# Kernel optimization log

Measured on AMD Instinct MI355X. Metric: run time of the kernel, lower is better.

The kernel has to match this reference:

```python
import jax, jax.numpy as jnp
from jax import lax
import numpy as np
from functools import reduce

# --- module hyperparameters (init_kwargs defaults) ---
T_LOW = 0.5; T_HIGH = 0.9; SIGMAS = (1.0, 2.0); BETA = 0.5
Z_RADIUS = 1; XY_RADIUS = 0; DUST_MIN_SIZE = 100; EPS = 1e-7
MAX_HYST_ITERS = 256   # flood-fill iteration cap (converges far earlier on real data)
MAX_CC_ITERS = 256     # label-propagation iteration cap


def _gauss_kernel(sigma):
    # separable gaussian, truncate at 3 sigma (standard scipy convention)
    r = int(3.0 * sigma + 0.5)
    x = np.arange(-r, r + 1, dtype=np.float32)
    k = np.exp(-(x * x) / (2.0 * sigma * sigma))
    return jnp.asarray(k / k.sum())


def _conv1d_axis(v, k, axis):
    # 'same' zero-padded 1D correlation along `axis` of a 3D volume
    r = k.shape[0] // 2
    pad = [(0, 0)] * 3; pad[axis] = (r, r)
    vp = jnp.pad(v, pad)
    n = v.shape[axis]
    out = jnp.zeros_like(v)
    for i in range(k.shape[0]):  # tiny fixed tap loop, vectorized over the volume
        sl = [slice(None)] * 3; sl[axis] = slice(i, i + n)
        out = out + k[i] * vp[tuple(sl)]
    return out


def _shifts6(x, pad_val):
    # 6-connected neighbor views (cross connectivity, matches ndi default)
    p = jnp.pad(x, 1, constant_values=pad_val)
    c = slice(1, -1)
    return (p[:-2, c, c], p[2:, c, c], p[c, :-2, c], p[c, 2:, c], p[c, c, :-2], p[c, c, 2:])


def _axis_morph(m, axis, radius, dilate):
    # box dilation/erosion along one axis (box SE is separable)
    op = jnp.logical_or if dilate else jnp.logical_and
    pad_val = (not dilate)
    for _ in range(radius):
        pad = [(1, 1) if a == axis else (0, 0) for a in range(3)]
        p = jnp.pad(m, pad, constant_values=pad_val)
        lo = tuple(slice(0, -2) if a == axis else slice(None) for a in range(3))
        hi = tuple(slice(2, None) if a == axis else slice(None) for a in range(3))
        m = op(op(m, p[lo]), p[hi])
    return m


def _hysteresis(vol):
    # keep low-threshold voxels connected to a high-threshold voxel (flood fill)
    low = vol > T_LOW
    high = vol > T_HIGH
    def body(st):
        m, _, i = st
        nm = m
        for s in _shifts6(m, False):
            nm = nm | s
        nm = nm & low
        return nm, jnp.any(nm != m), i + 1
    mask, _, _ = lax.while_loop(lambda st: st[1] & (st[2] < MAX_HYST_ITERS), body,
                                (high, jnp.bool_(True), jnp.int32(0)))
    return mask


def _closing(mask):
    # anisotropic binary closing with box SE (2*z_r+1, 2*xy_r+1, 2*xy_r+1)
    for axis, r in ((0, Z_RADIUS), (1, XY_RADIUS), (2, XY_RADIUS)):
        mask = _axis_morph(mask, axis, r, dilate=True)
    for axis, r in ((0, Z_RADIUS), (1, XY_RADIUS), (2, XY_RADIUS)):
        mask = _axis_morph(mask, axis, r, dilate=False)
    return mask


def _remove_small(mask):
    # connected-component labeling via max-label propagation, then size filter
    n = mask.size
    idx = jnp.arange(1, n + 1, dtype=jnp.int32).reshape(mask.shape)
    lab0 = jnp.where(mask, idx, 0)
    def body(st):
        l, _, i = st
        nl = l
        for s in _shifts6(l, 0):
            nl = jnp.maximum(nl, s)
        nl = jnp.where(mask, nl, 0)
        return nl, jnp.any(nl != l), i + 1
    lab, _, _ = lax.while_loop(lambda st: st[1] & (st[2] < MAX_CC_ITERS), body,
                               (lab0, jnp.bool_(True), jnp.int32(0)))
    counts = jax.ops.segment_sum(mask.ravel().astype(jnp.int32), lab.ravel(), num_segments=n + 1)
    return mask & (counts[lab] >= DUST_MIN_SIZE)


def _process_volume(v):
    d2 = jnp.asarray([1.0, -2.0, 1.0], v.dtype)
    surfs = []
    for sigma in SIGMAS:
        k = _gauss_kernel(sigma)
        s = v
        for ax in range(3):
            s = _conv1d_axis(s, k, ax)
        scale = sigma * sigma
        fxx = _conv1d_axis(s, d2, 0) * scale
        fyy = _conv1d_axis(s, d2, 1) * scale
        fzz = _conv1d_axis(s, d2, 2) * scale
        surf = jnp.exp(-(fxx * fxx + fyy * fyy) / (BETA * BETA * (fzz * fzz + EPS))) * jnp.abs(fzz)
        mx = surf.max()
        surfs.append(jnp.where(mx > 0, surf / (mx + EPS), jnp.zeros_like(surf)))
    surfaceness = reduce(jnp.maximum, surfs)  # max over sigma stack
    vol = lax.stop_gradient(v * surfaceness)  # binarization pipeline is piecewise constant
    mask = _hysteresis(vol)
    mask = _closing(mask)
    if DUST_MIN_SIZE > 0:
        mask = _remove_small(mask)
    return mask.astype(v.dtype)


def setup_inputs() -> dict:
    key = jax.random.key(0)
    outputs = jax.random.uniform(key, (2, 192, 192, 192), dtype=jnp.float32)
    return {"outputs": outputs}


def reference(outputs):
    return jax.vmap(_process_volume)(outputs)
```

## Files before the change

### kernel.cpp

```cpp
#include <hip/hip_runtime.h>
#include <cmath>

#define D3   192
#define SZP  (D3*D3)
#define NVOX (D3*D3*D3)
#define NTOT (2*NVOX)
#define NBLK (NTOT/256)
#define W3   (NTOT/64)
#define WBLK (W3/256)
#define NSUM (W3/64)
#define NQ   (NTOT/4)
#define NQB  (NQ/256)
#define BPB  (NVOX/256)

#define HT 16
#define HH 8
#define HL (HT+2*HH)
#define HLDS (HL*HL*3)
#define NHT  (12*12*2)

typedef unsigned long long u64;

struct Taps13 { float k[13]; };

__device__ __forceinline__ void coords(int idx, int& x, int& y, int& z, int& b) {
  x = idx % D3;
  y = (idx / D3) % D3;
  z = (idx / SZP) % D3;
  b = idx / NVOX;
}

template<int AXIS, int R>
__global__ void __launch_bounds__(256) conv1d_k(const float* __restrict__ in,
                                                float* __restrict__ out, Taps13 t) {
  int idx = blockIdx.x * 256 + threadIdx.x;
  int x, y, z, b; coords(idx, x, y, z, b);
  int c = (AXIS == 0) ? z : (AXIS == 1) ? y : x;
  const int stride = (AXIS == 0) ? SZP : (AXIS == 1) ? D3 : 1;
  float acc = 0.f;
#pragma unroll
  for (int i = -R; i <= R; ++i) {
    int cc = c + i;
    if (cc >= 0 && cc < D3)
      acc = __fadd_rn(acc, __fmul_rn(t.k[i + R], in[idx + i * stride]));
  }
  out[idx] = acc;
}

__global__ void __launch_bounds__(256) surf_k(const float* __restrict__ s,
                                              float* __restrict__ surf,
                                              float* __restrict__ bmax,
                                              float scale) {
  int idx = blockIdx.x * 256 + threadIdx.x;
  int x, y, z, b; coords(idx, x, y, z, b);
  float ctr = s[idx];
  float fxx, fyy, fzz;
  { float acc = 0.f;
    if (z > 0)      acc = __fadd_rn(acc, __fmul_rn(1.f, s[idx - SZP]));
    acc = __fadd_rn(acc, __fmul_rn(-2.f, ctr));
    if (z < D3 - 1) acc = __fadd_rn(acc, __fmul_rn(1.f, s[idx + SZP]));
    fxx = __fmul_rn(acc, scale); }
  { float acc = 0.f;
    if (y > 0)      acc = __fadd_rn(acc, __fmul_rn(1.f, s[idx - D3]));
    acc = __fadd_rn(acc, __fmul_rn(-2.f, ctr));
    if (y < D3 - 1) acc = __fadd_rn(acc, __fmul_rn(1.f, s[idx + D3]));
    fyy = __fmul_rn(acc, scale); }
  { float acc = 0.f;
    if (x > 0)      acc = __fadd_rn(acc, __fmul_rn(1.f, s[idx - 1]));
    acc = __fadd_rn(acc, __fmul_rn(-2.f, ctr));
    if (x < D3 - 1) acc = __fadd_rn(acc, __fmul_rn(1.f, s[idx + 1]));
    fzz = __fmul_rn(acc, scale); }

  float num = __fadd_rn(__fmul_rn(fxx, fxx), __fmul_rn(fyy, fyy));
  float den = __fmul_rn(0.25f, __fadd_rn(__fmul_rn(fzz, fzz), 1e-7f));
  float arg = __fdiv_rn(-num, den);
  float sv  = __fmul_rn(expf(arg), fabsf(fzz));
  surf[idx] = sv;

  float m = sv;
  #pragma unroll
  for (int off = 32; off > 0; off >>= 1) m = fmaxf(m, __shfl_down(m, off));
  __shared__ float wred[4];
  int lane = threadIdx.x & 63, wid = threadIdx.x >> 6;
  if (lane == 0) wred[wid] = m;
  __syncthreads();
  if (threadIdx.x == 0)
    bmax[blockIdx.x] = fmaxf(fmaxf(wred[0], wred[1]), fmaxf(wred[2], wred[3]));
}

__global__ void __launch_bounds__(256) reduce_max_k(const float* __restrict__ bmax,
                                                    unsigned int* __restrict__ mxp) {
  int b = blockIdx.x;
  const float* p = bmax + b * BPB;
  float m = 0.f;
  for (int i = threadIdx.x; i < BPB; i += 256) m = fmaxf(m, p[i]);
  #pragma unroll
  for (int off = 32; off > 0; off >>= 1) m = fmaxf(m, __shfl_down(m, off));
  __shared__ float wred[4];
  int lane = threadIdx.x & 63, wid = threadIdx.x >> 6;
  if (lane == 0) wred[wid] = m;
  __syncthreads();
  if (threadIdx.x == 0)
    mxp[b] = __float_as_uint(fmaxf(fmaxf(wred[0], wred[1]), fmaxf(wred[2], wred[3])));
}

__global__ void __launch_bounds__(256) mask_init_pack_k(const float* __restrict__ v,
                                                        const float* __restrict__ s1,
                                                        const float* __restrict__ s2,
                                                        const unsigned int* __restrict__ mx,
                                                        u64* __restrict__ lowW,
                                                        u64* __restrict__ mW) {
  int idx = blockIdx.x * 256 + threadIdx.x;
  int b = idx / NVOX;
  float m1 = __uint_as_float(mx[b]);
  float m2 = __uint_as_float(mx[2 + b]);
  float n1 = (m1 > 0.f) ? __fdiv_rn(s1[idx], __fadd_rn(m1, 1e-7f)) : 0.f;
  float n2 = (m2 > 0.f) ? __fdiv_rn(s2[idx], __fadd_rn(m2, 1e-7f)) : 0.f;
  float vol = __fmul_rn(v[idx], fmaxf(n1, n2));
  u64 bl = __ballot(vol > 0.5f);
  u64 bh = __ballot(vol > 0.9f);
  if ((threadIdx.x & 63) == 0) {
    lowW[idx >> 6] = bl;
    mW[idx >> 6]   = bh;
  }
}

__global__ void __launch_bounds__(256) hyst8_k(const u64* __restrict__ src,
                                               u64* __restrict__ dst,
                                               const u64* __restrict__ lowW,
                                               const int* __restrict__ fprev,
                                               int* __restrict__ fcur,
                                               int* __restrict__ chg, int iter) {
  if (iter > 0 && chg[iter - 1] == 0) return;
  const int r = blockIdx.x + 12 * blockIdx.y + 144 * blockIdx.z;
  if (iter > 0) {
    bool act = false;
    for (int dz = -1; dz <= 1 && !act; ++dz) {
      int zz = (int)blockIdx.y + dz; if (zz < 0 || zz >= 12) continue;
      for (int dy = -1; dy <= 1; ++dy) {
        int yy = (int)blockIdx.x + dy; if (yy < 0 || yy >= 12) continue;
        if (fprev[yy + 12 * zz + 144 * blockIdx.z]) { act = true; break; }
      }
    }
    if (!act) { if (threadIdx.x == 0) fcur[r] = 0; return; }
  }

  __shared__ u64 sA[HLDS], sB[HLDS];
  __shared__ int blkC;
  const int t = threadIdx.x;
  if (t == 0) blkC = 0;
  const int y0 = blockIdx.x * HT - HH;
  const int z0 = blockIdx.y * HT - HH;
  const int b  = blockIdx.z;

  u64 lowr[4][3], orig[4][3];
#pragma unroll
  for (int j = 0; j < 4; ++j) {
    int l = t + 256 * j;
    int yy = l & 31, zz = l >> 5;
    int y = y0 + yy, z = z0 + zz;
    bool in = (y >= 0 && y < D3 && z >= 0 && z < D3);
    int wb = 3 * y + 576 * z + 110592 * b;
#pragma unroll
    for (int xw = 0; xw < 3; ++xw) {
      u64 sv = in ? src[wb + xw]  : 0ull;
      u64 lv = in ? lowW[wb + xw] : 0ull;
      sA[l * 3 + xw] = sv;
      orig[j][xw] = sv;
      lowr[j][xw] = lv;
    }
  }
  __syncthreads();

  u64* cur = sA; u64* nxt = sB;
  for (int s = 0; s < 8; ++s) {
#pragma unroll
    for (int j = 0; j < 4; ++j) {
      int l = t + 256 * j;
      int yy = l & 31, zz = l >> 5;
      int base = l * 3;
      u64 w0 = cur[base], w1 = cur[base + 1], w2 = cur[base + 2];
      u64 n0 = w0 | (w0 << 1) | (w0 >> 1) | (w1 << 63);
      u64 n1 = w1 | (w1 << 1) | (w1 >> 1) | (w0 >> 63) | (w2 << 63);
      u64 n2 = w2 | (w2 << 1) | (w2 >> 1) | (w1 >> 63);
      if (yy > 0)  { n0 |= cur[base - 3];  n1 |= cur[base - 2];  n2 |= cur[base - 1]; }
      if (yy < 31) { n0 |= cur[base + 3];  n1 |= cur[base + 4];  n2 |= cur[base + 5]; }
      if (zz > 0)  { n0 |= cur[base - 96]; n1 |= cur[base - 95]; n2 |= cur[base - 94]; }
      if (zz < 31) { n0 |= cur[base + 96]; n1 |= cur[base + 97]; n2 |= cur[base + 98]; }
      nxt[base]     = n0 & lowr[j][0];
      nxt[base + 1] = n1 & lowr[j][1];
      nxt[base + 2] = n2 & lowr[j][2];
    }
    __syncthreads();
    u64* tmp = cur; cur = nxt; nxt = tmp;
  }

  bool ch = false;
#pragma unroll
  for (int j = 0; j < 4; ++j) {
    int l = t + 256 * j;
    int yy = l & 31, zz = l >> 5;
    if (yy >= HH && yy < HH + HT && zz >= HH && zz < HH + HT) {
      int y = y0 + yy, z = z0 + zz;
      int wb = 3 * y + 576 * z + 110592 * b;
#pragma unroll
      for (int xw = 0; xw < 3; ++xw) {
        u64 o = cur[l * 3 + xw];
        ch |= (o != orig[j][xw]);
        dst[wb + xw] = o;
      }
    }
  }
  if (ch) blkC = 1;
  __syncthreads();
  if (t == 0) { fcur[r] = blkC; if (blkC) chg[iter] = 1; }
}

__global__ void __launch_bounds__(256) close_z_k(const u64* __restrict__ mi,
                                                 u64* __restrict__ mo) {
  int w = blockIdx.x * 256 + threadIdx.x;
  int z = (w / 576) % D3;
  u64 c   = mi[w];
  u64 zm1 = (z > 0)      ? mi[w - 576]  : 0ull;
  u64 zm2 = (z > 1)      ? mi[w - 1152] : 0ull;
  u64 zp1 = (z < D3 - 1) ? mi[w + 576]  : 0ull;
  u64 zp2 = (z < D3 - 2) ? mi[w + 1152] : 0ull;
  u64 d0 = c | zm1 | zp1;
  u64 e  = d0;
  if (z > 0)      e &= (zm2 | zm1 | c);
  if (z < D3 - 1) e &= (c | zp1 | zp2);
  mo[w] = e;
}

__global__ void __launch_bounds__(256) label_init_k(const u64* __restrict__ closedW,
                                                    int* __restrict__ lab) {
  int idx = blockIdx.x * 256 + threadIdx.x;
  int bit = (int)((closedW[idx >> 6] >> (idx & 63)) & 1ull);
  lab[idx] = bit ? (idx % NVOX) + 1 : 0;
}

__device__ __forceinline__ int imax2(int a, int b) { return a > b ? a : b; }

__global__ void __launch_bounds__(256) cc_word_k(const int* __restrict__ src,
                                                 int* __restrict__ dst,
                                                 const u64* __restrict__ chgPrev,
                                                 u64* __restrict__ chgCur,
                                                 const u64* __restrict__ sumPrev,
                                                 u64* __restrict__ sumCur,
                                                 const u64* __restrict__ closedW,
                                                 int* __restrict__ chg, int iter) {
  if (iter > 0 && chg[iter - 1] == 0) return;
  __shared__ int blkC;
  if (threadIdx.x == 0) blkC = 0;
  __syncthreads();

  const int w = blockIdx.x * 256 + threadIdx.x;
  const int xw = w % 3;
  const int y  = (w / 3) % D3;
  const int z  = (w / 576) % D3;

  u64 F, U;
  if (iter == 0) {
    F = ~0ull; U = 0ull;
  } else {
    u64 c  = ((sumPrev[w >> 6] >> (w & 63)) & 1ull) ? chgPrev[w] : 0ull;
    u64 cl = 0ull, cr = 0ull, ym = 0ull, yp = 0ull, zm = 0ull, zp = 0ull;
    if (xw > 0      && ((sumPrev[(w - 1) >> 6]   >> ((w - 1) & 63))   & 1ull)) cl = chgPrev[w - 1];
    if (xw < 2      && ((sumPrev[(w + 1) >> 6]   >> ((w + 1) & 63))   & 1ull)) cr = chgPrev[w + 1];
    if (y > 0       && ((sumPrev[(w - 3) >> 6]   >> ((w - 3) & 63))   & 1ull)) ym = chgPrev[w - 3];
    if (y < D3 - 1  && ((sumPrev[(w + 3) >> 6]   >> ((w + 3) & 63))   & 1ull)) yp = chgPrev[w + 3];
    if (z > 0       && ((sumPrev[(w - 576) >> 6] >> ((w - 576) & 63)) & 1ull)) zm = chgPrev[w - 576];
    if (z < D3 - 1  && ((sumPrev[(w + 576) >> 6] >> ((w + 576) & 63)) & 1ull)) zp = chgPrev[w + 576];
    u64 nb = (c << 1) | (c >> 1) | (cl >> 63) | (cr << 63) | ym | yp | zm | zp;
    if ((nb | c) == 0ull) { F = 0ull; U = 0ull; }
    else {
      u64 cw = closedW[w];
      F = nb & cw;
      U = c & cw & ~F;
    }
  }

  u64 P = F | U;
  u64 newc = 0;
  if (P) {
    int idx0 = xw * 64 + D3 * y + SZP * z + (w / 110592) * NVOX;
#pragma unroll
    for (int q = 0; q < 16; ++q) {
      if (!((P >> (4 * q)) & 0xFull)) continue;
      int idx = idx0 + 4 * q;
      int4 s = *(const int4*)(src + idx);
      int4 o = s;
      if ((F >> (4 * q)) & 0xFull) {
        int x = xw * 64 + 4 * q;
        const int4 z4 = make_int4(0, 0, 0, 0);
        int4 yv = (y > 0)      ? *(const int4*)(src + idx - D3)  : z4;
        int4 yw = (y < D3 - 1) ? *(const int4*)(src + idx + D3)  : z4;
        int4 zv = (z > 0)      ? *(const int4*)(src + idx - SZP) : z4;
        int4 zw = (z < D3 - 1) ? *(const int4*)(src + idx + SZP) : z4;
        int lf = (x > 0)       ? src[idx - 1] : 0;
        int rt = (x < D3 - 4)  ? src[idx + 4] : 0;
        o.x = s.x ? imax2(imax2(imax2(s.x, lf),  imax2(s.y, yv.x)), imax2(imax2(yw.x, zv.x), zw.x)) : 0;
        o.y = s.y ? imax2(imax2(imax2(s.y, s.x), imax2(s.z, yv.y)), imax2(imax2(yw.y, zv.y), zw.y)) : 0;
        o.z = s.z ? imax2(imax2(imax2(s.z, s.y), imax2(s.w, yv.z)), imax2(imax2(yw.z, zv.z), zw.z)) : 0;
        o.w = s.w ? imax2(imax2(imax2(s.w, s.z), imax2(rt,  yv.w)), imax2(imax2(yw.w, zv.w), zw.w)) : 0;
      }
      *(int4*)(dst + idx) = o;
      u64 df = (u64)((o.x != s.x) | ((o.y != s.y) << 1) |
                     ((o.z != s.z) << 2) | ((o.w != s.w) << 3));
      newc |= df << (4 * q);
    }
  }

  u64 bal = __ballot(newc != 0ull);
  if (newc) chgCur[w] = newc;
  if ((threadIdx.x & 63) == 0) sumCur[w >> 6] = bal;
  if (bal) blkC = 1;
  __syncthreads();
  if (threadIdx.x == 0 && blkC) chg[iter] = 1;
}

__global__ void __launch_bounds__(256) count_k(const int* __restrict__ lab,
                                               unsigned int* __restrict__ counts) {
  int q = blockIdx.x * 256 + threadIdx.x;
  int idx = q << 2;
  int b = idx / NVOX;
  int4 L = *(const int4*)(lab + idx);
  unsigned int* cb = counts + b * NVOX;
  if (L.x > 0) atomicAdd(&cb[L.x - 1], 1u);
  if (L.y > 0) atomicAdd(&cb[L.y - 1], 1u);
  if (L.z > 0) atomicAdd(&cb[L.z - 1], 1u);
  if (L.w > 0) atomicAdd(&cb[L.w - 1], 1u);
}

__global__ void __launch_bounds__(256) final_k(const int* __restrict__ lab,
                                               const unsigned int* __restrict__ counts,
                                               float* __restrict__ out) {
  int q = blockIdx.x * 256 + threadIdx.x;
  int idx = q << 2;
  int b = idx / NVOX;
  int4 L = *(const int4*)(lab + idx);
  const unsigned int* cb = counts + b * NVOX;
  float4 rr;
  rr.x = (L.x > 0 && cb[L.x - 1] >= 100u) ? 1.f : 0.f;
  rr.y = (L.y > 0 && cb[L.y - 1] >= 100u) ? 1.f : 0.f;
  rr.z = (L.z > 0 && cb[L.z - 1] >= 100u) ? 1.f : 0.f;
  rr.w = (L.w > 0 && cb[L.w - 1] >= 100u) ? 1.f : 0.f;
  *(float4*)(out + idx) = rr;
}

static float np_sum_f32(const float* a, int n) {
  if (n < 8) { float res = 0.f; for (int i = 0; i < n; i++) res += a[i]; return res; }
  float r[8]; for (int j = 0; j < 8; j++) r[j] = a[j];
  int i = 8;
  for (; i < n - (n % 8); i += 8) for (int j = 0; j < 8; j++) r[j] += a[i + j];
  float res = ((r[0] + r[1]) + (r[2] + r[3])) + ((r[4] + r[5]) + (r[6] + r[7]));
  for (; i < n; i++) res += a[i];
  return res;
}

extern "C" void kernel_launch(void* const* d_in, const int* in_sizes, int n_in,
                              void* d_out, int out_size, void* d_ws, size_t ws_size,
                              hipStream_t stream) {
  const float* v = (const float*)d_in[0];
  float* out = (float*)d_out;
  char* base = (char*)d_ws;
  const size_t SZBUF = (size_t)NTOT * 4;
  const size_t SZW   = (size_t)W3 * 8;

  float* A  = (float*)base;
  float* Cf = (float*)(base + SZBUF);
  unsigned int* mx = (unsigned int*)(base + 2 * SZBUF);
  float* bmax = (float*)(base + 2 * SZBUF + 256);
  float* Bf = (float*)d_out;

  u64* lowW    = (u64*)base;
  u64* mWA     = (u64*)(base + SZW);
  u64* mWB     = (u64*)(base + 2 * SZW);
  u64* closedW = (u64*)(base + 3 * SZW);
  u64* chgWA   = (u64*)(base + 4 * SZW);
  u64* chgWB   = (u64*)(base + 5 * SZW);
  u64* sumA    = (u64*)(base + 6 * SZW);
  u64* sumB    = sumA + NSUM;
  int* chgH = (int*)(sumB + NSUM);
  int* chgC = chgH + 32;
  int* hF0  = chgC + 256;
  int* hF1  = hF0 + NHT;

  int* labA = (int*)Bf;
  int* labB = (int*)Cf;
  unsigned int* counts = (unsigned int*)Cf;

  dim3 g(NBLK), gw(WBLK), gq(NQB), blk(256);

  const double sigmas[2] = {1.0, 2.0};
  for (int si = 0; si < 2; ++si) {
    double sigma = sigmas[si];
    int r = (int)(3.0 * sigma + 0.5);
    int n = 2 * r + 1;
    float a[13], k[13];
    for (int i = 0; i < n; i++) {
      float xx = (float)(i - r);
      float t  = xx * xx;
      float arg = -(t) / (float)(2.0 * sigma * sigma);
      a[i] = (float)std::exp((double)arg);
    }
    float ssum = np_sum_f32(a, n);
    for (int i = 0; i < n; i++) k[i] = a[i] / ssum;

    Taps13 T = {};
    for (int i = 0; i < n; i++) T.k[i] = k[i];
    float scale = (float)(sigma * sigma);
    float* starget = (si == 0) ? Cf : Bf;

    if (r == 3) {
      conv1d_k<0, 3><<<g, blk, 0, stream>>>(v,  A,  T);
      conv1d_k<1, 3><<<g, blk, 0, stream>>>(A,  Bf, T);
      conv1d_k<2, 3><<<g, blk, 0, stream>>>(Bf, A,  T);
    } else {
      conv1d_k<0, 6><<<g, blk, 0, stream>>>(v,  A,  T);
      conv1d_k<1, 6><<<g, blk, 0, stream>>>(A,  Bf, T);
      conv1d_k<2, 6><<<g, blk, 0, stream>>>(Bf, A,  T);
    }
    surf_k<<<g, blk, 0, stream>>>(A, starget, bmax, scale);
    reduce_max_k<<<dim3(2), blk, 0, stream>>>(bmax, mx + 2 * si);
  }

  hipMemsetAsync(chgH, 0, (32 + 256) * 4, stream);
  mask_init_pack_k<<<g, blk, 0, stream>>>(v, Cf, Bf, mx, lowW, mWA);

  for (int it = 0; it < 32; ++it) {
    const u64* s = (it & 1) ? mWB : mWA;
    u64*       d = (it & 1) ? mWA : mWB;
    const int* fp = (it & 1) ? hF0 : hF1;
    int*       fc = (it & 1) ? hF1 : hF0;
    hyst8_k<<<dim3(12, 12, 2), blk, 0, stream>>>(s, d, lowW, fp, fc, chgH, it);
  }

  close_z_k<<<gw, blk, 0, stream>>>(mWA, closedW);

  label_init_k<<<g, blk, 0, stream>>>(closedW, labA);
  for (int it = 0; it < 256; ++it) {
    const int* s = (it & 1) ? labB : labA;
    int*       d = (it & 1) ? labA : labB;
    const u64* cp = (it & 1) ? chgWB : chgWA;
    u64*       cc = (it & 1) ? chgWA : chgWB;
    const u64* sp = (it & 1) ? sumB : sumA;
    u64*       sc = (it & 1) ? sumA : sumB;
    cc_word_k<<<gw, blk, 0, stream>>>(s, d, cp, cc, sp, sc, closedW, chgC, it);
  }

  hipMemsetAsync(counts, 0, SZBUF, stream);
  count_k<<<gq, blk, 0, stream>>>(labA, counts);
  final_k<<<gq, blk, 0, stream>>>(labA, counts, out);
}
```

Before: 1.867 ms.

## Fuse hysteresis, closing, labeling and dust removal into one persistent cooperative kernel

Replaces the roughly 290 per-iteration kernel launches for hysteresis, z-closing, label init, connected-component propagation, counting and final masking with a single cooperative persistent kernel of 256 blocks. Phases are separated by a hand-written flag-based grid barrier, and the loops exit early once an iteration reports no change. The closing is fused into label init, so the closedW buffer and its mask in the CC step are dropped. This removes launch and early-return overhead but limits parallelism to 256 blocks, which loop over tiles and words, and adds global-barrier latency per iteration.

```diff
diff --git a/kernel.cpp b/kernel.cpp
--- a/kernel.cpp
+++ b/kernel.cpp
@@ -7,7 +7,7 @@
 #define NTOT (2*NVOX)
 #define NBLK (NTOT/256)
 #define W3   (NTOT/64)
-#define WBLK (W3/256)
+#define WGRP (W3/256)
 #define NSUM (W3/64)
 #define NQ   (NTOT/4)
 #define NQB  (NQ/256)
@@ -18,6 +18,9 @@
 #define HL (HT+2*HH)
 #define HLDS (HL*HL*3)
 #define NHT  (12*12*2)
+
+#define GBLK 256
+#define TT   (GBLK*256)
 
 typedef unsigned long long u64;
 
@@ -125,227 +128,274 @@
   }
 }
 
-__global__ void __launch_bounds__(256) hyst8_k(const u64* __restrict__ src,
-                                               u64* __restrict__ dst,
-                                               const u64* __restrict__ lowW,
-                                               const int* __restrict__ fprev,
-                                               int* __restrict__ fcur,
-                                               int* __restrict__ chg, int iter) {
-  if (iter > 0 && chg[iter - 1] == 0) return;
-  const int r = blockIdx.x + 12 * blockIdx.y + 144 * blockIdx.z;
-  if (iter > 0) {
-    bool act = false;
-    for (int dz = -1; dz <= 1 && !act; ++dz) {
-      int zz = (int)blockIdx.y + dz; if (zz < 0 || zz >= 12) continue;
-      for (int dy = -1; dy <= 1; ++dy) {
-        int yy = (int)blockIdx.x + dy; if (yy < 0 || yy >= 12) continue;
-        if (fprev[yy + 12 * zz + 144 * blockIdx.z]) { act = true; break; }
-      }
+struct Flag { int v; int pad[15]; };
+
+struct PipeArgs {
+  const u64* lowW; u64* mWA; u64* mWB;
+  int* labA; int* labB;
+  u64* chgWA; u64* chgWB; u64* sumA; u64* sumB;
+  int* chgH; int* chgC; int* hF0; int* hF1;
+  Flag* arr; int* go;
+  float* outp;
+};
+
+__device__ __forceinline__ int imax2(int a, int b) { return a > b ? a : b; }
+
+__device__ __forceinline__ void gbar(Flag* arr, int* go, int rnd) {
+  __syncthreads();
+  if (threadIdx.x == 0) {
+    __threadfence();
+    __hip_atomic_store(&arr[blockIdx.x].v, rnd, __ATOMIC_RELEASE, __HIP_MEMORY_SCOPE_AGENT);
+  }
+  if (blockIdx.x == 0) {
+    while (__hip_atomic_load(&arr[threadIdx.x].v, __ATOMIC_ACQUIRE,
+                             __HIP_MEMORY_SCOPE_AGENT) < rnd)
+      __builtin_amdgcn_s_sleep(1);
+    __syncthreads();
+    if (threadIdx.x == 0) {
+      __threadfence();
+      __hip_atomic_store(go, rnd, __ATOMIC_RELEASE, __HIP_MEMORY_SCOPE_AGENT);
     }
-    if (!act) { if (threadIdx.x == 0) fcur[r] = 0; return; }
-  }
-
+  } else if (threadIdx.x == 0) {
+    while (__hip_atomic_load(go, __ATOMIC_ACQUIRE, __HIP_MEMORY_SCOPE_AGENT) < rnd)
+      __builtin_amdgcn_s_sleep(1);
+  }
+  __syncthreads();
+}
+
+__global__ void __launch_bounds__(256, 1) pipeline_k(PipeArgs a) {
   __shared__ u64 sA[HLDS], sB[HLDS];
   __shared__ int blkC;
   const int t = threadIdx.x;
-  if (t == 0) blkC = 0;
-  const int y0 = blockIdx.x * HT - HH;
-  const int z0 = blockIdx.y * HT - HH;
-  const int b  = blockIdx.z;
-
-  u64 lowr[4][3], orig[4][3];
-#pragma unroll
-  for (int j = 0; j < 4; ++j) {
-    int l = t + 256 * j;
-    int yy = l & 31, zz = l >> 5;
-    int y = y0 + yy, z = z0 + zz;
-    bool in = (y >= 0 && y < D3 && z >= 0 && z < D3);
-    int wb = 3 * y + 576 * z + 110592 * b;
-#pragma unroll
-    for (int xw = 0; xw < 3; ++xw) {
-      u64 sv = in ? src[wb + xw]  : 0ull;
-      u64 lv = in ? lowW[wb + xw] : 0ull;
-      sA[l * 3 + xw] = sv;
-      orig[j][xw] = sv;
-      lowr[j][xw] = lv;
+  const int gtid = blockIdx.x * 256 + t;
+  int rnd = 0;
+
+  u64* hsrc = a.mWA; u64* hdst = a.mWB;
+  int* fp = a.hF1;   int* fc = a.hF0;
+  for (int it = 0; it < 32; ++it) {
+    for (int vt = blockIdx.x; vt < NHT; vt += GBLK) {
+      int tyi = vt % 12, tzi = (vt / 12) % 12, tb = vt / 144;
+      bool act = true;
+      if (it > 0) {
+        act = false;
+        for (int dz = -1; dz <= 1 && !act; ++dz) {
+          int zz = tzi + dz; if (zz < 0 || zz >= 12) continue;
+          for (int dy = -1; dy <= 1; ++dy) {
+            int yy = tyi + dy; if (yy < 0 || yy >= 12) continue;
+            if (fp[yy + 12 * zz + 144 * tb]) { act = true; break; }
+          }
+        }
+      }
+      if (!act) { if (t == 0) fc[vt] = 0; continue; }
+
+      if (t == 0) blkC = 0;
+      __syncthreads();
+      const int y0 = tyi * HT - HH;
+      const int z0 = tzi * HT - HH;
+
+      u64 lowr[4][3], orig[4][3];
+#pragma unroll
+      for (int j = 0; j < 4; ++j) {
+        int l = t + 256 * j;
+        int yy = l & 31, zz = l >> 5;
+        int y = y0 + yy, z = z0 + zz;
+        bool in = (y >= 0 && y < D3 && z >= 0 && z < D3);
+        int wb = 3 * y + 576 * z + 110592 * tb;
+#pragma unroll
+        for (int xw = 0; xw < 3; ++xw) {
+          u64 sv = in ? hsrc[wb + xw]   : 0ull;
+          u64 lv = in ? a.lowW[wb + xw] : 0ull;
+          sA[l * 3 + xw] = sv;
+          orig[j][xw] = sv;
+          lowr[j][xw] = lv;
+        }
+      }
+      __syncthreads();
+
+      u64* cur = sA; u64* nxt = sB;
+      for (int s = 0; s < 8; ++s) {
+#pragma unroll
+        for (int j = 0; j < 4; ++j) {
+          int l = t + 256 * j;
+          int yy = l & 31, zz = l >> 5;
+          int base = l * 3;
+          u64 w0 = cur[base], w1 = cur[base + 1], w2 = cur[base + 2];
+          u64 n0 = w0 | (w0 << 1) | (w0 >> 1) | (w1 << 63);
+          u64 n1 = w1 | (w1 << 1) | (w1 >> 1) | (w0 >> 63) | (w2 << 63);
+          u64 n2 = w2 | (w2 << 1) | (w2 >> 1) | (w1 >> 63);
+          if (yy > 0)  { n0 |= cur[base - 3];  n1 |= cur[base - 2];  n2 |= cur[base - 1]; }
+          if (yy < 31) { n0 |= cur[base + 3];  n1 |= cur[base + 4];  n2 |= cur[base + 5]; }
+          if (zz > 0)  { n0 |= cur[base - 96]; n1 |= cur[base - 95]; n2 |= cur[base - 94]; }
+          if (zz < 31) { n0 |= cur[base + 96]; n1 |= cur[base + 97]; n2 |= cur[base + 98]; }
+          nxt[base]     = n0 & lowr[j][0];
+          nxt[base + 1] = n1 & lowr[j][1];
+          nxt[base + 2] = n2 & lowr[j][2];
+        }
+        __syncthreads();
+        u64* tmp = cur; cur = nxt; nxt = tmp;
+      }
+
+      bool ch = false;
+#pragma unroll
+      for (int j = 0; j < 4; ++j) {
+        int l = t + 256 * j;
+        int yy = l & 31, zz = l >> 5;
+        if (yy >= HH && yy < HH + HT && zz >= HH && zz < HH + HT) {
+          int y = y0 + yy, z = z0 + zz;
+          int wb = 3 * y + 576 * z + 110592 * tb;
+#pragma unroll
+          for (int xw = 0; xw < 3; ++xw) {
+            u64 o = cur[l * 3 + xw];
+            ch |= (o != orig[j][xw]);
+            hdst[wb + xw] = o;
+          }
+        }
+      }
+      if (ch) blkC = 1;
+      __syncthreads();
+      if (t == 0) {
+        fc[vt] = blkC;
+        if (blkC) __hip_atomic_store(&a.chgH[it], 1, __ATOMIC_RELAXED, __HIP_MEMORY_SCOPE_AGENT);
+      }
     }
-  }
-  __syncthreads();
-
-  u64* cur = sA; u64* nxt = sB;
-  for (int s = 0; s < 8; ++s) {
-#pragma unroll
-    for (int j = 0; j < 4; ++j) {
-      int l = t + 256 * j;
-      int yy = l & 31, zz = l >> 5;
-      int base = l * 3;
-      u64 w0 = cur[base], w1 = cur[base + 1], w2 = cur[base + 2];
-      u64 n0 = w0 | (w0 << 1) | (w0 >> 1) | (w1 << 63);
-      u64 n1 = w1 | (w1 << 1) | (w1 >> 1) | (w0 >> 63) | (w2 << 63);
-      u64 n2 = w2 | (w2 << 1) | (w2 >> 1) | (w1 >> 63);
-      if (yy > 0)  { n0 |= cur[base - 3];  n1 |= cur[base - 2];  n2 |= cur[base - 1]; }
-      if (yy < 31) { n0 |= cur[base + 3];  n1 |= cur[base + 4];  n2 |= cur[base + 5]; }
-      if (zz > 0)  { n0 |= cur[base - 96]; n1 |= cur[base - 95]; n2 |= cur[base - 94]; }
-      if (zz < 31) { n0 |= cur[base + 96]; n1 |= cur[base + 97]; n2 |= cur[base + 98]; }
-      nxt[base]     = n0 & lowr[j][0];
-      nxt[base + 1] = n1 & lowr[j][1];
-      nxt[base + 2] = n2 & lowr[j][2];
+    gbar(a.arr, a.go, ++rnd);
+    { u64* tm = hsrc; hsrc = hdst; hdst = tm; }
+    { int* ti = fp; fp = fc; fc = ti; }
+    if (a.chgH[it] == 0) break;
+  }
+
+  for (int q = gtid; q < NQ; q += TT) {
+    int idx = q << 2;
+    int w = idx >> 6, sh = idx & 63;
+    int z = (w / 576) % D3;
+    u64 c   = hsrc[w];
+    u64 zm1 = (z > 0)      ? hsrc[w - 576]  : 0ull;
+    u64 zm2 = (z > 1)      ? hsrc[w - 1152] : 0ull;
+    u64 zp1 = (z < D3 - 1) ? hsrc[w + 576]  : 0ull;
+    u64 zp2 = (z < D3 - 2) ? hsrc[w + 1152] : 0ull;
+    u64 e = c | zm1 | zp1;
+    if (z > 0)      e &= (zm2 | zm1 | c);
+    if (z < D3 - 1) e &= (c | zp1 | zp2);
+    unsigned bits = (unsigned)((e >> sh) & 0xFull);
+    int rel = idx % NVOX;
+    int4 L;
+    L.x = (bits & 1u) ? rel + 1 : 0;
+    L.y = (bits & 2u) ? rel + 2 : 0;
+    L.z = (bits & 4u) ? rel + 3 : 0;
+    L.w = (bits & 8u) ? rel + 4 : 0;
+    *(int4*)(a.labA + idx) = L;
+  }
+  gbar(a.arr, a.go, ++rnd);
+
+  int* cs = a.labA; int* cd = a.labB;
+  u64* cp = a.chgWA; u64* cn = a.chgWB;
+  u64* sp = a.sumA;  u64* sn = a.sumB;
+  for (int it = 0; it < 256; ++it) {
+    for (int vb = blockIdx.x; vb < WGRP; vb += GBLK) {
+      const int w = vb * 256 + t;
+      const int xw = w % 3;
+      const int y  = (w / 3) % D3;
+      const int z  = (w / 576) % D3;
+
+      u64 F, U;
+      if (it == 0) {
+        F = ~0ull; U = 0ull;
+      } else {
+        u64 c  = ((sp[w >> 6] >> (w & 63)) & 1ull) ? cp[w] : 0ull;
+        u64 cl = 0ull, cr = 0ull, ym = 0ull, yp = 0ull, zm = 0ull, zp = 0ull;
+        if (xw > 0      && ((sp[(w - 1) >> 6]   >> ((w - 1) & 63))   & 1ull)) cl = cp[w - 1];
+        if (xw < 2      && ((sp[(w + 1) >> 6]   >> ((w + 1) & 63))   & 1ull)) cr = cp[w + 1];
+        if (y > 0       && ((sp[(w - 3) >> 6]   >> ((w - 3) & 63))   & 1ull)) ym = cp[w - 3];
+        if (y < D3 - 1  && ((sp[(w + 3) >> 6]   >> ((w + 3) & 63))   & 1ull)) yp = cp[w + 3];
+        if (z > 0       && ((sp[(w - 576) >> 6] >> ((w - 576) & 63)) & 1ull)) zm = cp[w - 576];
+        if (z < D3 - 1  && ((sp[(w + 576) >> 6] >> ((w + 576) & 63)) & 1ull)) zp = cp[w + 576];
+        u64 nb = (c << 1) | (c >> 1) | (cl >> 63) | (cr << 63) | ym | yp | zm | zp;
+        if ((nb | c) == 0ull) { F = 0ull; U = 0ull; }
+        else {
+          F = nb; U = c & ~nb;
+        }
+      }
+
+      u64 P = F | U;
+      u64 newc = 0;
+      if (P) {
+        int idx0 = xw * 64 + D3 * y + SZP * z + (w / 110592) * NVOX;
+#pragma unroll
+        for (int q = 0; q < 16; ++q) {
+          if (!((P >> (4 * q)) & 0xFull)) continue;
+          int idx = idx0 + 4 * q;
+          int4 s = *(const int4*)(cs + idx);
+          int4 o = s;
+          if ((F >> (4 * q)) & 0xFull) {
+            int x = xw * 64 + 4 * q;
+            const int4 z4 = make_int4(0, 0, 0, 0);
+            int4 yv = (y > 0)      ? *(const int4*)(cs + idx - D3)  : z4;
+            int4 yw = (y < D3 - 1) ? *(const int4*)(cs + idx + D3)  : z4;
+            int4 zv = (z > 0)      ? *(const int4*)(cs + idx - SZP) : z4;
+            int4 zw = (z < D3 - 1) ? *(const int4*)(cs + idx + SZP) : z4;
+            int lf = (x > 0)       ? cs[idx - 1] : 0;
+            int rt = (x < D3 - 4)  ? cs[idx + 4] : 0;
+            o.x = s.x ? imax2(imax2(imax2(s.x, lf),  imax2(s.y, yv.x)), imax2(imax2(yw.x, zv.x), zw.x)) : 0;
+            o.y = s.y ? imax2(imax2(imax2(s.y, s.x), imax2(s.z, yv.y)), imax2(imax2(yw.y, zv.y), zw.y)) : 0;
+            o.z = s.z ? imax2(imax2(imax2(s.z, s.y), imax2(s.w, yv.z)), imax2(imax2(yw.z, zv.z), zw.z)) : 0;
+            o.w = s.w ? imax2(imax2(imax2(s.w, s.z), imax2(rt,  yv.w)), imax2(imax2(yw.w, zv.w), zw.w)) : 0;
+          }
+          *(int4*)(cd + idx) = o;
+          u64 df = (u64)((o.x != s.x) | ((o.y != s.y) << 1) |
+                         ((o.z != s.z) << 2) | ((o.w != s.w) << 3));
+          newc |= df << (4 * q);
+        }
+      }
+
+      u64 bal = __ballot(newc != 0ull);
+      if (newc) cn[w] = newc;
+      if ((t & 63) == 0) {
+        sn[w >> 6] = bal;
+        if (bal) __hip_atomic_store(&a.chgC[it], 1, __ATOMIC_RELAXED, __HIP_MEMORY_SCOPE_AGENT);
+      }
     }
-    __syncthreads();
-    u64* tmp = cur; cur = nxt; nxt = tmp;
-  }
-
-  bool ch = false;
-#pragma unroll
-  for (int j = 0; j < 4; ++j) {
-    int l = t + 256 * j;
-    int yy = l & 31, zz = l >> 5;
-    if (yy >= HH && yy < HH + HT && zz >= HH && zz < HH + HT) {
-      int y = y0 + yy, z = z0 + zz;
-      int wb = 3 * y + 576 * z + 110592 * b;
-#pragma unroll
-      for (int xw = 0; xw < 3; ++xw) {
-        u64 o = cur[l * 3 + xw];
-        ch |= (o != orig[j][xw]);
-        dst[wb + xw] = o;
-      }
-    }
-  }
-  if (ch) blkC = 1;
-  __syncthreads();
-  if (t == 0) { fcur[r] = blkC; if (blkC) chg[iter] = 1; }
-}
-
-__global__ void __launch_bounds__(256) close_z_k(const u64* __restrict__ mi,
-                                                 u64* __restrict__ mo) {
-  int w = blockIdx.x * 256 + threadIdx.x;
-  int z = (w / 576) % D3;
-  u64 c   = mi[w];
-  u64 zm1 = (z > 0)      ? mi[w - 576]  : 0ull;
-  u64 zm2 = (z > 1)      ? mi[w - 1152] : 0ull;
-  u64 zp1 = (z < D3 - 1) ? mi[w + 576]  : 0ull;
-  u64 zp2 = (z < D3 - 2) ? mi[w + 1152] : 0ull;
-  u64 d0 = c | zm1 | zp1;
-  u64 e  = d0;
-  if (z > 0)      e &= (zm2 | zm1 | c);
-  if (z < D3 - 1) e &= (c | zp1 | zp2);
-  mo[w] = e;
-}
-
-__global__ void __launch_bounds__(256) label_init_k(const u64* __restrict__ closedW,
-                                                    int* __restrict__ lab) {
-  int idx = blockIdx.x * 256 + threadIdx.x;
-  int bit = (int)((closedW[idx >> 6] >> (idx & 63)) & 1ull);
-  lab[idx] = bit ? (idx % NVOX) + 1 : 0;
-}
-
-__device__ __forceinline__ int imax2(int a, int b) { return a > b ? a : b; }
-
-__global__ void __launch_bounds__(256) cc_word_k(const int* __restrict__ src,
-                                                 int* __restrict__ dst,
-                                                 const u64* __restrict__ chgPrev,
-                                                 u64* __restrict__ chgCur,
-                                                 const u64* __restrict__ sumPrev,
-                                                 u64* __restrict__ sumCur,
-                                                 const u64* __restrict__ closedW,
-                                                 int* __restrict__ chg, int iter) {
-  if (iter > 0 && chg[iter - 1] == 0) return;
-  __shared__ int blkC;
-  if (threadIdx.x == 0) blkC = 0;
-  __syncthreads();
-
-  const int w = blockIdx.x * 256 + threadIdx.x;
-  const int xw = w % 3;
-  const int y  = (w / 3) % D3;
-  const int z  = (w / 576) % D3;
-
-  u64 F, U;
-  if (iter == 0) {
-    F = ~0ull; U = 0ull;
-  } else {
-    u64 c  = ((sumPrev[w >> 6] >> (w & 63)) & 1ull) ? chgPrev[w] : 0ull;
-    u64 cl = 0ull, cr = 0ull, ym = 0ull, yp = 0ull, zm = 0ull, zp = 0ull;
-    if (xw > 0      && ((sumPrev[(w - 1) >> 6]   >> ((w - 1) & 63))   & 1ull)) cl = chgPrev[w - 1];
-    if (xw < 2      && ((sumPrev[(w + 1) >> 6]   >> ((w + 1) & 63))   & 1ull)) cr = chgPrev[w + 1];
-    if (y > 0       && ((sumPrev[(w - 3) >> 6]   >> ((w - 3) & 63))   & 1ull)) ym = chgPrev[w - 3];
-    if (y < D3 - 1  && ((sumPrev[(w + 3) >> 6]   >> ((w + 3) & 63))   & 1ull)) yp = chgPrev[w + 3];
-    if (z > 0       && ((sumPrev[(w - 576) >> 6] >> ((w - 576) & 63)) & 1ull)) zm = chgPrev[w - 576];
-    if (z < D3 - 1  && ((sumPrev[(w + 576) >> 6] >> ((w + 576) & 63)) & 1ull)) zp = chgPrev[w + 576];
-    u64 nb = (c << 1) | (c >> 1) | (cl >> 63) | (cr << 63) | ym | yp | zm | zp;
-    if ((nb | c) == 0ull) { F = 0ull; U = 0ull; }
-    else {
-      u64 cw = closedW[w];
-      F = nb & cw;
-      U = c & cw & ~F;
-    }
-  }
-
-  u64 P = F | U;
-  u64 newc = 0;
-  if (P) {
-    int idx0 = xw * 64 + D3 * y + SZP * z + (w / 110592) * NVOX;
-#pragma unroll
-    for (int q = 0; q < 16; ++q) {
-      if (!((P >> (4 * q)) & 0xFull)) continue;
-      int idx = idx0 + 4 * q;
-      int4 s = *(const int4*)(src + idx);
-      int4 o = s;
-      if ((F >> (4 * q)) & 0xFull) {
-        int x = xw * 64 + 4 * q;
-        const int4 z4 = make_int4(0, 0, 0, 0);
-        int4 yv = (y > 0)      ? *(const int4*)(src + idx - D3)  : z4;
-        int4 yw = (y < D3 - 1) ? *(const int4*)(src + idx + D3)  : z4;
-        int4 zv = (z > 0)      ? *(const int4*)(src + idx - SZP) : z4;
-        int4 zw = (z < D3 - 1) ? *(const int4*)(src + idx + SZP) : z4;
-        int lf = (x > 0)       ? src[idx - 1] : 0;
-        int rt = (x < D3 - 4)  ? src[idx + 4] : 0;
-        o.x = s.x ? imax2(imax2(imax2(s.x, lf),  imax2(s.y, yv.x)), imax2(imax2(yw.x, zv.x), zw.x)) : 0;
-        o.y = s.y ? imax2(imax2(imax2(s.y, s.x), imax2(s.z, yv.y)), imax2(imax2(yw.y, zv.y), zw.y)) : 0;
-        o.z = s.z ? imax2(imax2(imax2(s.z, s.y), imax2(s.w, yv.z)), imax2(imax2(yw.z, zv.z), zw.z)) : 0;
-        o.w = s.w ? imax2(imax2(imax2(s.w, s.z), imax2(rt,  yv.w)), imax2(imax2(yw.w, zv.w), zw.w)) : 0;
-      }
-      *(int4*)(dst + idx) = o;
-      u64 df = (u64)((o.x != s.x) | ((o.y != s.y) << 1) |
-                     ((o.z != s.z) << 2) | ((o.w != s.w) << 3));
-      newc |= df << (4 * q);
-    }
-  }
-
-  u64 bal = __ballot(newc != 0ull);
-  if (newc) chgCur[w] = newc;
-  if ((threadIdx.x & 63) == 0) sumCur[w >> 6] = bal;
-  if (bal) blkC = 1;
-  __syncthreads();
-  if (threadIdx.x == 0 && blkC) chg[iter] = 1;
-}
-
-__global__ void __launch_bounds__(256) count_k(const int* __restrict__ lab,
-                                               unsigned int* __restrict__ counts) {
-  int q = blockIdx.x * 256 + threadIdx.x;
-  int idx = q << 2;
-  int b = idx / NVOX;
-  int4 L = *(const int4*)(lab + idx);
-  unsigned int* cb = counts + b * NVOX;
-  if (L.x > 0) atomicAdd(&cb[L.x - 1], 1u);
-  if (L.y > 0) atomicAdd(&cb[L.y - 1], 1u);
-  if (L.z > 0) atomicAdd(&cb[L.z - 1], 1u);
-  if (L.w > 0) atomicAdd(&cb[L.w - 1], 1u);
-}
-
-__global__ void __launch_bounds__(256) final_k(const int* __restrict__ lab,
-                                               const unsigned int* __restrict__ counts,
-                                               float* __restrict__ out) {
-  int q = blockIdx.x * 256 + threadIdx.x;
-  int idx = q << 2;
-  int b = idx / NVOX;
-  int4 L = *(const int4*)(lab + idx);
-  const unsigned int* cb = counts + b * NVOX;
-  float4 rr;
-  rr.x = (L.x > 0 && cb[L.x - 1] >= 100u) ? 1.f : 0.f;
-  rr.y = (L.y > 0 && cb[L.y - 1] >= 100u) ? 1.f : 0.f;
-  rr.z = (L.z > 0 && cb[L.z - 1] >= 100u) ? 1.f : 0.f;
-  rr.w = (L.w > 0 && cb[L.w - 1] >= 100u) ? 1.f : 0.f;
-  *(float4*)(out + idx) = rr;
+    gbar(a.arr, a.go, ++rnd);
+    { int* ti = cs; cs = cd; cd = ti; }
+    { u64* tm = cp; cp = cn; cn = tm; }
+    { u64* tm = sp; sp = sn; sn = tm; }
+    if (a.chgC[it] == 0) break;
+  }
+
+  if (cs != a.labA) {
+    for (int q = gtid; q < NQ; q += TT)
+      *(int4*)(a.labA + (q << 2)) = *(const int4*)(cs + (q << 2));
+    gbar(a.arr, a.go, ++rnd);
+  }
+
+  unsigned int* counts = (unsigned int*)a.labB;
+  for (int q = gtid; q < NQ; q += TT)
+    *(int4*)((int*)counts + (q << 2)) = make_int4(0, 0, 0, 0);
+  gbar(a.arr, a.go, ++rnd);
+
+  for (int q = gtid; q < NQ; q += TT) {
+    int idx = q << 2;
+    int b = idx / NVOX;
+    int4 L = *(const int4*)(a.labA + idx);
+    unsigned int* cb = counts + (size_t)b * NVOX;
+    if (L.x > 0) atomicAdd(&cb[L.x - 1], 1u);
+    if (L.y > 0) atomicAdd(&cb[L.y - 1], 1u);
+    if (L.z > 0) atomicAdd(&cb[L.z - 1], 1u);
+    if (L.w > 0) atomicAdd(&cb[L.w - 1], 1u);
+  }
+  gbar(a.arr, a.go, ++rnd);
+
+  for (int q = gtid; q < NQ; q += TT) {
+    int idx = q << 2;
+    int b = idx / NVOX;
+    int4 L = *(const int4*)(a.labA + idx);
+    const unsigned int* cb = counts + (size_t)b * NVOX;
+    float4 rr;
+    rr.x = (L.x > 0 && cb[L.x - 1] >= 100u) ? 1.f : 0.f;
+    rr.y = (L.y > 0 && cb[L.y - 1] >= 100u) ? 1.f : 0.f;
+    rr.z = (L.z > 0 && cb[L.z - 1] >= 100u) ? 1.f : 0.f;
+    rr.w = (L.w > 0 && cb[L.w - 1] >= 100u) ? 1.f : 0.f;
+    *(float4*)(a.outp + idx) = rr;
+  }
 }
 
 static float np_sum_f32(const float* a, int n) {
@@ -373,24 +423,25 @@
   float* bmax = (float*)(base + 2 * SZBUF + 256);
   float* Bf = (float*)d_out;
 
-  u64* lowW    = (u64*)base;
-  u64* mWA     = (u64*)(base + SZW);
-  u64* mWB     = (u64*)(base + 2 * SZW);
-  u64* closedW = (u64*)(base + 3 * SZW);
-  u64* chgWA   = (u64*)(base + 4 * SZW);
-  u64* chgWB   = (u64*)(base + 5 * SZW);
-  u64* sumA    = (u64*)(base + 6 * SZW);
-  u64* sumB    = sumA + NSUM;
-  int* chgH = (int*)(sumB + NSUM);
-  int* chgC = chgH + 32;
-  int* hF0  = chgC + 256;
-  int* hF1  = hF0 + NHT;
+  u64* lowW  = (u64*)base;
+  u64* mWA   = (u64*)(base + SZW);
+  u64* mWB   = (u64*)(base + 2 * SZW);
+  u64* chgWA = (u64*)(base + 3 * SZW);
+  u64* chgWB = (u64*)(base + 4 * SZW);
+  u64* sumA  = (u64*)(base + 5 * SZW);
+  u64* sumB  = sumA + NSUM;
+  int* chgH  = (int*)(sumB + NSUM);
+  int* chgC  = chgH + 32;
+  int* hF0   = chgC + 256;
+  int* hF1   = hF0 + NHT;
+  Flag* arr  = (Flag*)(hF1 + NHT);
+  int* go    = (int*)(arr + GBLK);
+  size_t ctrlBytes = (char*)(go + 16) - (char*)chgH;
 
   int* labA = (int*)Bf;
   int* labB = (int*)Cf;
-  unsigned int* counts = (unsigned int*)Cf;
-
-  dim3 g(NBLK), gw(WBLK), gq(NQB), blk(256);
+
+  dim3 g(NBLK), blk(256);
 
   const double sigmas[2] = {1.0, 2.0};
   for (int si = 0; si < 2; ++si) {
@@ -425,31 +476,12 @@
     reduce_max_k<<<dim3(2), blk, 0, stream>>>(bmax, mx + 2 * si);
   }
 
-  hipMemsetAsync(chgH, 0, (32 + 256) * 4, stream);
+  hipMemsetAsync(chgH, 0, ctrlBytes, stream);
   mask_init_pack_k<<<g, blk, 0, stream>>>(v, Cf, Bf, mx, lowW, mWA);
 
-  for (int it = 0; it < 32; ++it) {
-    const u64* s = (it & 1) ? mWB : mWA;
-    u64*       d = (it & 1) ? mWA : mWB;
-    const int* fp = (it & 1) ? hF0 : hF1;
-    int*       fc = (it & 1) ? hF1 : hF0;
-    hyst8_k<<<dim3(12, 12, 2), blk, 0, stream>>>(s, d, lowW, fp, fc, chgH, it);
-  }
-
-  close_z_k<<<gw, blk, 0, stream>>>(mWA, closedW);
-
-  label_init_k<<<g, blk, 0, stream>>>(closedW, labA);
-  for (int it = 0; it < 256; ++it) {
-    const int* s = (it & 1) ? labB : labA;
-    int*       d = (it & 1) ? labA : labB;
-    const u64* cp = (it & 1) ? chgWB : chgWA;
-    u64*       cc = (it & 1) ? chgWA : chgWB;
-    const u64* sp = (it & 1) ? sumB : sumA;
-    u64*       sc = (it & 1) ? sumA : sumB;
-    cc_word_k<<<gw, blk, 0, stream>>>(s, d, cp, cc, sp, sc, closedW, chgC, it);
-  }
-
-  hipMemsetAsync(counts, 0, SZBUF, stream);
-  count_k<<<gq, blk, 0, stream>>>(labA, counts);
-  final_k<<<gq, blk, 0, stream>>>(labA, counts, out);
-}
+  PipeArgs pa{lowW, mWA, mWB, labA, labB, chgWA, chgWB, sumA, sumB,
+              chgH, chgC, hF0, hF1, arr, go, out};
+  void* args[] = {&pa};
+  hipLaunchCooperativeKernel((const void*)pipeline_k, dim3(GBLK), dim3(256),
+                             args, 0, stream);
+}
```

Result: slower. 4.274 ms (+128.9%).

## Replace tail of label propagation with LDS-tiled multi-step CC kernel gated by activity flags

Applied to the files above, without the earlier changes.

Keeps only 12 global word-level label-propagation passes, then projects the change bitmaps onto 32x8x8 regions. It finishes with up to 61 launches of a new kernel. Each launch loads a haloed 40x16x16 tile into shared memory, runs up to 4 propagation steps locally, and skips tiles whose neighborhood had no changes. This cuts the many global-memory passes of the 256-iteration loop. Correctness depends on the fixed iteration caps covering convergence, since 12 + 61*4 steps is roughly the old budget but with different gating semantics, and the counts buffer is moved to another workspace region.

```diff
diff --git a/kernel.cpp b/kernel.cpp
--- a/kernel.cpp
+++ b/kernel.cpp
@@ -18,6 +18,13 @@
 #define HL (HT+2*HH)
 #define HLDS (HL*HL*3)
 #define NHT  (12*12*2)
+
+#define CRX 40
+#define CRY 16
+#define CRZ 16
+#define CRN (CRX*CRY*CRZ)
+#define CJ  (CRN/256)
+#define NCT (6*24*24*2)
 
 typedef unsigned long long u64;
 
@@ -319,13 +326,120 @@
   if (threadIdx.x == 0 && blkC) chg[iter] = 1;
 }
 
+__global__ void __launch_bounds__(256) proj_k(const u64* __restrict__ chgW,
+                                              const u64* __restrict__ sumW,
+                                              int* __restrict__ freg) {
+  int reg = blockIdx.x * 4 + (threadIdx.x >> 6);
+  int lane = threadIdx.x & 63;
+  int bx = reg % 6; int t2 = reg / 6;
+  int by = t2 % 24; int t3 = t2 / 24;
+  int bz = t3 % 24; int b = t3 / 24;
+  int ly = lane & 7, lz = lane >> 3;
+  int y = by * 8 + ly, z = bz * 8 + lz;
+  int w = (bx >> 1) + 3 * y + 576 * z + 110592 * b;
+  u64 m = ((sumW[w >> 6] >> (w & 63)) & 1ull) ? chgW[w] : 0ull;
+  u64 mask = (bx & 1) ? 0xFFFFFFFF00000000ull : 0x00000000FFFFFFFFull;
+  u64 bal = __ballot((m & mask) != 0ull);
+  if (lane == 0) freg[reg] = (bal != 0ull) ? 1 : 0;
+}
+
+__global__ void __launch_bounds__(256) cc4_k(const int* __restrict__ src,
+                                             int* __restrict__ dst,
+                                             const int* __restrict__ fprev,
+                                             int* __restrict__ fcur,
+                                             const int* __restrict__ gate,
+                                             int* __restrict__ setf) {
+  if (*gate == 0) return;
+  const int bx = blockIdx.x, by = blockIdx.y;
+  const int bz = blockIdx.z % 24, b = blockIdx.z / 24;
+  const int r = bx + 6 * by + 144 * bz + 3456 * b;
+
+  bool act = false;
+  for (int dz = -1; dz <= 1 && !act; ++dz) {
+    int zz = bz + dz; if (zz < 0 || zz >= 24) continue;
+    for (int dy = -1; dy <= 1 && !act; ++dy) {
+      int yy = by + dy; if (yy < 0 || yy >= 24) continue;
+      for (int dx = -1; dx <= 1; ++dx) {
+        int xx = bx + dx; if (xx < 0 || xx >= 6) continue;
+        if (fprev[xx + 6 * yy + 144 * zz + 3456 * b]) { act = true; break; }
+      }
+    }
+  }
+  if (!act) { if (threadIdx.x == 0) fcur[r] = 0; return; }
+
+  __shared__ int sL[CRN];
+  __shared__ int chStep;
+  const int t = threadIdx.x;
+  const int gx0 = bx * 32 - 4, gy0 = by * 8 - 4, gz0 = bz * 8 - 4;
+
+  u64 mxlo = 0, mxhi = 0, mylo = 0, myhi = 0, mzlo = 0, mzhi = 0;
+  int val[CJ];
+#pragma unroll
+  for (int j = 0; j < CJ; ++j) {
+    int l = t + 256 * j;
+    int x = l % CRX; int rr = l / CRX; int y = rr % CRY; int z = rr / CRY;
+    int gx = gx0 + x, gy = gy0 + y, gz = gz0 + z;
+    int vv = 0;
+    if (gx >= 0 && gx < D3 && gy >= 0 && gy < D3 && gz >= 0 && gz < D3)
+      vv = src[gx + D3 * gy + SZP * gz + b * NVOX];
+    sL[l] = vv;
+    val[j] = vv;
+    mxlo |= ((u64)(x > 0))       << j;  mxhi |= ((u64)(x < CRX - 1)) << j;
+    mylo |= ((u64)(y > 0))       << j;  myhi |= ((u64)(y < CRY - 1)) << j;
+    mzlo |= ((u64)(z > 0))       << j;  mzhi |= ((u64)(z < CRZ - 1)) << j;
+  }
+
+  bool anyC = false;
+  for (int s = 0; s < 4; ++s) {
+    if (t == 0) chStep = 0;
+    __syncthreads();
+    bool ch = false;
+#pragma unroll
+    for (int j = 0; j < CJ; ++j) {
+      int l = t + 256 * j;
+      int vv = sL[l];
+      int o = vv;
+      if (vv > 0) {
+        if ((mxlo >> j) & 1) o = imax2(o, sL[l - 1]);
+        if ((mxhi >> j) & 1) o = imax2(o, sL[l + 1]);
+        if ((mylo >> j) & 1) o = imax2(o, sL[l - CRX]);
+        if ((myhi >> j) & 1) o = imax2(o, sL[l + CRX]);
+        if ((mzlo >> j) & 1) o = imax2(o, sL[l - CRX * CRY]);
+        if ((mzhi >> j) & 1) o = imax2(o, sL[l + CRX * CRY]);
+        ch |= (o != vv);
+      }
+      val[j] = o;
+    }
+    if (ch) chStep = 1;
+    __syncthreads();
+    if (chStep == 0) break;
+    anyC = true;
+#pragma unroll
+    for (int j = 0; j < CJ; ++j) {
+      int l = t + 256 * j;
+      if (val[j] != 0) sL[l] = val[j];
+    }
+  }
+
+#pragma unroll
+  for (int j = 0; j < CJ; ++j) {
+    int l = t + 256 * j;
+    int x = l % CRX; int rr = l / CRX; int y = rr % CRY; int z = rr / CRY;
+    if (x >= 4 && x < 36 && y >= 4 && y < 12 && z >= 4 && z < 12) {
+      int gx = gx0 + x, gy = gy0 + y, gz = gz0 + z;
+      dst[gx + D3 * gy + SZP * gz + b * NVOX] = val[j];
+    }
+  }
+  if (t == 0) { fcur[r] = anyC ? 1 : 0; if (anyC) *setf = 1; }
+}
+
 __global__ void __launch_bounds__(256) count_k(const int* __restrict__ lab,
                                                unsigned int* __restrict__ counts) {
   int q = blockIdx.x * 256 + threadIdx.x;
   int idx = q << 2;
   int b = idx / NVOX;
   int4 L = *(const int4*)(lab + idx);
-  unsigned int* cb = counts + b * NVOX;
+  unsigned int* cb = counts + (size_t)b * NVOX;
   if (L.x > 0) atomicAdd(&cb[L.x - 1], 1u);
   if (L.y > 0) atomicAdd(&cb[L.y - 1], 1u);
   if (L.z > 0) atomicAdd(&cb[L.z - 1], 1u);
@@ -339,7 +453,7 @@
   int idx = q << 2;
   int b = idx / NVOX;
   int4 L = *(const int4*)(lab + idx);
-  const unsigned int* cb = counts + b * NVOX;
+  const unsigned int* cb = counts + (size_t)b * NVOX;
   float4 rr;
   rr.x = (L.x > 0 && cb[L.x - 1] >= 100u) ? 1.f : 0.f;
   rr.y = (L.y > 0 && cb[L.y - 1] >= 100u) ? 1.f : 0.f;
@@ -381,14 +495,18 @@
   u64* chgWB   = (u64*)(base + 5 * SZW);
   u64* sumA    = (u64*)(base + 6 * SZW);
   u64* sumB    = sumA + NSUM;
-  int* chgH = (int*)(sumB + NSUM);
-  int* chgC = chgH + 32;
-  int* hF0  = chgC + 256;
-  int* hF1  = hF0 + NHT;
+  int* chgH   = (int*)(sumB + NSUM);
+  int* chgC   = chgH + 32;
+  int* hF0    = chgC + 256;
+  int* hF1    = hF0 + NHT;
+  int* cF0    = hF1 + NHT;
+  int* cF1    = cF0 + NCT;
+  int* cc4chg = cF1 + NCT;
+  size_t ctrlBytes = (char*)(cc4chg + 64) - (char*)chgH;
 
   int* labA = (int*)Bf;
   int* labB = (int*)Cf;
-  unsigned int* counts = (unsigned int*)Cf;
+  unsigned int* counts = (unsigned int*)base;
 
   dim3 g(NBLK), gw(WBLK), gq(NQB), blk(256);
 
@@ -425,7 +543,7 @@
     reduce_max_k<<<dim3(2), blk, 0, stream>>>(bmax, mx + 2 * si);
   }
 
-  hipMemsetAsync(chgH, 0, (32 + 256) * 4, stream);
+  hipMemsetAsync(chgH, 0, ctrlBytes, stream);
   mask_init_pack_k<<<g, blk, 0, stream>>>(v, Cf, Bf, mx, lowW, mWA);
 
   for (int it = 0; it < 32; ++it) {
@@ -439,7 +557,7 @@
   close_z_k<<<gw, blk, 0, stream>>>(mWA, closedW);
 
   label_init_k<<<g, blk, 0, stream>>>(closedW, labA);
-  for (int it = 0; it < 256; ++it) {
+  for (int it = 0; it < 12; ++it) {
     const int* s = (it & 1) ? labB : labA;
     int*       d = (it & 1) ? labA : labB;
     const u64* cp = (it & 1) ? chgWB : chgWA;
@@ -449,7 +567,18 @@
     cc_word_k<<<gw, blk, 0, stream>>>(s, d, cp, cc, sp, sc, closedW, chgC, it);
   }
 
+  proj_k<<<dim3(NCT / 4), blk, 0, stream>>>(chgWA, sumA, cF0);
+
+  for (int j = 0; j < 61; ++j) {
+    const int* s = (j & 1) ? labB : labA;
+    int*       d = (j & 1) ? labA : labB;
+    const int* fp = (j & 1) ? cF1 : cF0;
+    int*       fc = (j & 1) ? cF0 : cF1;
+    const int* gate = (j == 0) ? &chgC[11] : &cc4chg[j - 1];
+    cc4_k<<<dim3(6, 24, 48), blk, 0, stream>>>(s, d, fp, fc, gate, &cc4chg[j]);
+  }
+
   hipMemsetAsync(counts, 0, SZBUF, stream);
-  count_k<<<gq, blk, 0, stream>>>(labA, counts);
-  final_k<<<gq, blk, 0, stream>>>(labA, counts, out);
-}
+  count_k<<<gq, blk, 0, stream>>>(labB, counts);
+  final_k<<<gq, blk, 0, stream>>>(labB, counts, out);
+}
```

Result: slower. 2.474 ms (+32.5%).
